# Performance work log

Hardware: AMD Instinct MI355X
Metric: run time of the kernel (lower is better)

The kernel has to match this reference:

```python
import jax, jax.numpy as jnp
import numpy as np

B, T, N, D = 8, 32, 24, 128          # batch, seq_len, max_node_num, roi_feature_size
H_LINK, H_LSTM, C, P = 128, 128, 6, 3  # link hidden, lstm hidden, big_attr_classes, propagate_layers


def setup_inputs() -> dict:
    key = jax.random.key(0)
    ks = jax.random.split(key, 20)
    node_num_rec = jax.random.randint(ks[0], (B, T), 2, N + 1)  # valid nodes per frame
    node_mask = jnp.arange(N)[None, None, :] < node_num_rec[:, :, None]          # [B,T,N]
    pair_mask = node_mask[:, :, :, None] & node_mask[:, :, None, :]              # [B,T,N,N]
    offdiag = ~jnp.eye(N, dtype=bool)
    # post-ResNet ROI features; invalid nodes / self-edges are zero (as in the torch code)
    node_resnet = jax.random.normal(ks[1], (B, T, D, N)) * node_mask[:, :, None, :]
    edge_resnet = jax.random.normal(ks[2], (B, T, D, N, N)) * (pair_mask & offdiag)[:, :, None]

    def w(k, shape, fan):
        return jax.random.normal(k, shape) / np.sqrt(fan)

    return dict(
        node_resnet=node_resnet, edge_resnet=edge_resnet,
        link_W1=w(ks[3], (H_LINK, D), D), link_b1=jnp.zeros((H_LINK,)),
        link_W2=w(ks[4], (1, H_LINK), H_LINK), link_b2=jnp.zeros((1,)),
        msg_Wh=w(ks[5], (D, D), 2 * D), msg_We=w(ks[6], (D, D), 2 * D), msg_b=jnp.zeros((D,)),
        gru_Wih=w(ks[7], (3 * D, D), D), gru_Whh=w(ks[8], (3 * D, D), D),
        gru_bih=jnp.zeros((3 * D,)), gru_bhh=jnp.zeros((3 * D,)),
        lstm_Wih=w(ks[9], (4 * H_LSTM, D), D), lstm_Whh=w(ks[10], (4 * H_LSTM, H_LSTM), H_LSTM),
        lstm_bih=jnp.zeros((4 * H_LSTM,)), lstm_bhh=jnp.zeros((4 * H_LSTM,)),
        ro_W=w(ks[11], (C, H_LSTM), H_LSTM), ro_b=jnp.zeros((C,)),
        node_num_rec=node_num_rec,
    )


def reference(node_resnet, edge_resnet, link_W1, link_b1, link_W2, link_b2,
              msg_Wh, msg_We, msg_b, gru_Wih, gru_Whh, gru_bih, gru_bhh,
              lstm_Wih, lstm_Whh, lstm_bih, lstm_bhh, ro_W, ro_b, node_num_rec):
    node_mask = jnp.arange(N)[None, None, :] < node_num_rec[:, :, None]      # [B,T,N]
    pair_mask = node_mask[:, :, :, None] & node_mask[:, :, None, :]          # [B,T,N,N]
    fmask_n = node_mask[:, :, None, :].astype(node_resnet.dtype)             # [B,T,1,N]
    fmask_p = pair_mask.astype(node_resnet.dtype)                            # [B,T,N,N]

    h_node = node_resnet      # [B,T,D,N]
    h_edge = edge_resnet      # [B,T,D,N,N]
    for _ in range(P):
        # link_fun (GraphConv = per-edge 1x1-conv MLP) -> adjacency logits, sigmoid gate on valid pairs
        hid = jax.nn.relu(jnp.einsum('btdvw,hd->bthvw', h_edge, link_W1)
                          + link_b1[None, None, :, None, None])
        adj = jnp.einsum('bthvw,h->btvw', hid, link_W2[0]) + link_b2[0]      # [B,T,N,N]
        gate = jax.nn.sigmoid(adj) * fmask_p
        # message_fun 'linear_concat_relu': relu(W @ concat(h_w, e_vw) + b), e_vw is raw edge feature
        msg = jax.nn.relu(jnp.einsum('btdw,od->btow', h_node, msg_Wh)[:, :, :, None, :]
                          + jnp.einsum('btdvw,od->btovw', edge_resnet, msg_We)
                          + msg_b[None, None, :, None, None])                # [B,T,D,N,N]
        gated = gate[:, :, None] * msg
        # hidden edge states of next round: gated messages in valid region, clone of edge feats elsewhere
        h_edge = jnp.where(pair_mask[:, :, None], gated, edge_resnet)
        m_v = jnp.sum(gated, axis=-1)                                        # [B,T,D,N] sum over senders
        # update_fun: single-step GRU, input m_v, hidden h_node
        x = m_v.transpose(0, 1, 3, 2)      # [B,T,N,D]
        h = h_node.transpose(0, 1, 3, 2)
        gi = x @ gru_Wih.T + gru_bih
        gh = h @ gru_Whh.T + gru_bhh
        i_r, i_z, i_n = jnp.split(gi, 3, axis=-1)
        h_r, h_z, h_n = jnp.split(gh, 3, axis=-1)
        r = jax.nn.sigmoid(i_r + h_r)
        z = jax.nn.sigmoid(i_z + h_z)
        n = jnp.tanh(i_n + r * h_n)
        h_new = ((1.0 - z) * n + z * h).transpose(0, 1, 3, 2)                # [B,T,D,N]
        h_node = jnp.where(node_mask[:, :, None, :], h_new, node_resnet)

    # temporal LSTM over seq dim; node (and batch) axis acts as LSTM batch, zero initial state
    x_seq = h_node.transpose(1, 0, 3, 2).reshape(T, B * N, D)
    h0 = jnp.zeros((B * N, H_LSTM), dtype=x_seq.dtype)
    c0 = jnp.zeros_like(h0)

    def cell(carry, xt):
        h, c = carry
        g = xt @ lstm_Wih.T + lstm_bih + h @ lstm_Whh.T + lstm_bhh
        i, f, gg, o = jnp.split(g, 4, axis=-1)
        c = jax.nn.sigmoid(f) * c + jax.nn.sigmoid(i) * jnp.tanh(gg)
        h = jax.nn.sigmoid(o) * jnp.tanh(c)
        return (h, c), h

    _, out = jax.lax.scan(cell, (h0, c0), x_seq)                             # [T,B*N,H]
    out = out.reshape(T, B, N, H_LSTM).transpose(1, 0, 2, 3)                 # [B,T,N,H]
    pred_label = (out @ ro_W.T + ro_b) * node_mask[..., None]                # [B,T,N,C]
    return pred_label
```

## Files before the change

### kernel.cpp

```cpp
#include <hip/hip_runtime.h>
#include <cmath>

typedef unsigned short u16;
typedef unsigned int   u32;
typedef short bf16x8 __attribute__((ext_vector_type(8)));
typedef float f32x4 __attribute__((ext_vector_type(4)));

constexpr int B_ = 8, T_ = 32, N_ = 24, D_ = 128;
constexpr int BT_ = B_ * T_;
constexpr int VW_ = N_ * N_;
constexpr int BTN_ = BT_ * N_;
constexpr int BTVW_ = BT_ * VW_;
constexpr int P_ = 3;
constexpr int C_ = 6;
constexpr int SA_ = 136;

__device__ __forceinline__ float bits2f(u32 u) { float f; __builtin_memcpy(&f, &u, 4); return f; }
__device__ __forceinline__ float bf2f(u16 h) { return bits2f(((u32)h) << 16); }
__device__ __forceinline__ u16 f2bf(float f) {
    u32 u; __builtin_memcpy(&u, &f, 4);
    u32 r = u + 0x7FFFu + ((u >> 16) & 1u);
    return (u16)(r >> 16);
}
__device__ __forceinline__ f32x4 ld4bf(const u16* p) {
    const uint2 v = *(const uint2*)p;
    f32x4 r;
    r[0] = bf2f((u16)v.x); r[1] = bf2f((u16)(v.x >> 16));
    r[2] = bf2f((u16)v.y); r[3] = bf2f((u16)(v.y >> 16));
    return r;
}
__device__ __forceinline__ float fexp2(float x) { return __builtin_amdgcn_exp2f(x); }
__device__ __forceinline__ float frcp(float x) { return __builtin_amdgcn_rcpf(x); }
__device__ __forceinline__ float sigm(float x) {
    return frcp(1.0f + fexp2(x * -1.4426950408889634f));
}
__device__ __forceinline__ float ftanh(float x) {
    const float t = fexp2(fabsf(x) * -2.8853900817779268f);
    return copysignf((1.0f - t) * frcp(1.0f + t), x);
}

struct CvtArgs {
    const void* src[10];
    u16* dst[10];
    int start[11];
};

__global__ __launch_bounds__(256) void k_convall(CvtArgs a) {
    const int idx = blockIdx.x * 256 + threadIdx.x;
    if (idx >= a.start[10]) return;
    int s = 0;
#pragma unroll
    for (int i = 1; i < 10; ++i) s += (idx >= a.start[i]) ? 1 : 0;
    const int off = idx - a.start[s];
    a.dst[s][off] = f2bf(((const float*)a.src[s])[off]);
}

struct FlArgs {
    const float* src[7];
    u16* dst[7];
    int start[8];
};

__global__ __launch_bounds__(256) void k_fraglin(FlArgs a) {
    const int idx = blockIdx.x * 256 + threadIdx.x;
    if (idx >= a.start[7]) return;
    int s = 0;
#pragma unroll
    for (int i = 1; i < 7; ++i) s += (idx >= a.start[i]) ? 1 : 0;
    const int off = idx - a.start[s];
    const int e = off & 7, lane = (off >> 3) & 63;
    const int ks = (off >> 9) & 3, rb = off >> 11;
    const int m = lane & 15, quad = lane >> 4;
    a.dst[s][off] = f2bf(a.src[s][(size_t)(rb * 16 + m) * 128 + ks * 32 + quad * 8 + e]);
}

__global__ __launch_bounds__(256) void k_transpose_node(const float* __restrict__ node,
                                                        float* __restrict__ HN,
                                                        u16* __restrict__ HNb) {
    const int bt = blockIdx.x;
    for (int f = threadIdx.x; f < 3072; f += 256) {
        const int d = f / 24, n = f - d * 24;
        const float v = node[(size_t)bt * 3072 + f];
        HN[(size_t)bt * 3072 + n * 128 + d] = v;
        HNb[(size_t)bt * 3072 + n * 128 + d] = f2bf(v);
    }
}

__global__ __launch_bounds__(64, 4) void k_prep(
    const float* __restrict__ edge, const u16* __restrict__ WeF,
    const u16* __restrict__ W1F, const u16* __restrict__ b1,
    const u16* __restrict__ W2, const u16* __restrict__ b2,
    u16* __restrict__ ME, float* __restrict__ ADJ) {
    __shared__ __align__(16) u16 A[32 * 128];
    const int tid = threadIdx.x;
    const int bt = blockIdx.x / 18, tile = blockIdx.x % 18;
    const int vw0 = tile * 32;
    const size_t ebase = (size_t)bt * D_ * VW_ + vw0;
    const int vq = tid & 7, dg = tid >> 3;
    u32* A32 = (u32*)A;
    {
        float4 fa[8], fb[8];
#pragma unroll
        for (int it = 0; it < 8; ++it) {
            const int d0 = it * 16 + dg * 2;
            fa[it] = *(const float4*)&edge[ebase + (size_t)d0 * VW_ + vq * 4];
            fb[it] = *(const float4*)&edge[ebase + (size_t)(d0 + 1) * VW_ + vq * 4];
        }
#pragma unroll
        for (int it = 0; it < 8; ++it) {
            const int d0 = it * 16 + dg * 2;
            const float* pa = (const float*)&fa[it];
            const float* pb = (const float*)&fb[it];
#pragma unroll
            for (int i = 0; i < 4; ++i) {
                const int row = vq * 4 + i;
                const int sw32 = ((row >> 2) & 7) * 4;
                A32[row * 64 + ((d0 >> 1) ^ sw32)] =
                    (u32)f2bf(pa[i]) | ((u32)f2bf(pb[i]) << 16);
            }
        }
    }
    __syncthreads();
    const int m = tid & 15, quad = tid >> 4;
    bf16x8 a[2][4];
#pragma unroll
    for (int rt = 0; rt < 2; ++rt) {
        const int row = rt * 16 + m;
        const int sw16 = ((row >> 2) & 7) * 8;
#pragma unroll
        for (int ks = 0; ks < 4; ++ks)
            a[rt][ks] = *(const bf16x8*)&A[row * 128 + ((ks * 32 + quad * 8) ^ sw16)];
    }
    const f32x4 z = {0.f, 0.f, 0.f, 0.f};
    float p[2][4] = {};
    const float b2v = bf2f(b2[0]);
#pragma unroll
    for (int ct = 0; ct < 8; ++ct) {
        bf16x8 bwe[4], bw1[4];
#pragma unroll
        for (int ks = 0; ks < 4; ++ks) {
            bwe[ks] = *(const bf16x8*)&WeF[((ct * 4 + ks) << 9) + tid * 8];
            bw1[ks] = *(const bf16x8*)&W1F[((ct * 4 + ks) << 9) + tid * 8];
        }
        f32x4 accE[2], accA[2];
#pragma unroll
        for (int rt = 0; rt < 2; ++rt) { accE[rt] = z; accA[rt] = z; }
#pragma unroll
        for (int rt = 0; rt < 2; ++rt)
#pragma unroll
            for (int ks = 0; ks < 4; ++ks) {
                accE[rt] = __builtin_amdgcn_mfma_f32_16x16x32_bf16(bwe[ks], a[rt][ks], accE[rt], 0, 0, 0);
                accA[rt] = __builtin_amdgcn_mfma_f32_16x16x32_bf16(a[rt][ks], bw1[ks], accA[rt], 0, 0, 0);
            }
#pragma unroll
        for (int rt = 0; rt < 2; ++rt) {
            const u32 lo = (u32)f2bf(accE[rt][0]) | ((u32)f2bf(accE[rt][1]) << 16);
            const u32 hi = (u32)f2bf(accE[rt][2]) | ((u32)f2bf(accE[rt][3]) << 16);
            *(uint2*)&ME[(size_t)(bt * VW_ + vw0 + rt * 16 + m) * 128 + ct * 16 + quad * 4] =
                make_uint2(lo, hi);
        }
        const int n = ct * 16 + m;
        const float b1v = bf2f(b1[n]);
        const float w2v = bf2f(W2[n]);
#pragma unroll
        for (int rt = 0; rt < 2; ++rt)
#pragma unroll
            for (int reg = 0; reg < 4; ++reg)
                p[rt][reg] += fmaxf(accA[rt][reg] + b1v, 0.0f) * w2v;
    }
#pragma unroll
    for (int rt = 0; rt < 2; ++rt)
#pragma unroll
        for (int reg = 0; reg < 4; ++reg) {
            float v = p[rt][reg];
            v += __shfl_xor(v, 1);
            v += __shfl_xor(v, 2);
            v += __shfl_xor(v, 4);
            v += __shfl_xor(v, 8);
            p[rt][reg] = v;
        }
    if (m == 0) {
#pragma unroll
        for (int rt = 0; rt < 2; ++rt)
#pragma unroll
            for (int reg = 0; reg < 4; ++reg)
                ADJ[bt * VW_ + vw0 + rt * 16 + quad * 4 + reg] = p[rt][reg] + b2v;
    }
}

template <bool ADJP>
__global__ __launch_bounds__(256) void k_fused(
    const u16* __restrict__ ME, const float* __restrict__ XW,
    const u16* __restrict__ mb,
    const u16* __restrict__ W1F, const u16* __restrict__ b1,
    const u16* __restrict__ W2, const u16* __restrict__ b2,
    const int* __restrict__ nnr, float* __restrict__ ADJ,
    u16* __restrict__ MVb) {
    __shared__ __align__(16) u16 A[48 * SA_];
    __shared__ float gate_s[48];
    __shared__ float2 mvp[2][2][64];
    const int tid = threadIdx.x;
    const int blk = blockIdx.x;
    const int bt = blk / 12, pr = blk - bt * 12;
    const int v0 = pr * 2;
    const int e0 = bt * VW_ + v0 * N_;
    const int nv = nnr[bt];

    if (tid < 48) gate_s[tid] = sigm(ADJ[e0 + tid]);
    __syncthreads();
    {
        const int op = tid & 63;
        const int sub = (tid >> 6) & 1;
        const int grp = tid >> 7;
        const int v = v0 + grp;
        const u32 mbu = ((const u32*)mb)[op];
        const float mb0 = bf2f((u16)mbu), mb1 = bf2f((u16)(mbu >> 16));
        const bool vva = v < nv;
        u32 meR[12]; float2 xwR[12];
#pragma unroll
        for (int i = 0; i < 12; ++i) {
            const int w = sub * 12 + i;
            const int rr = grp * 24 + w;
            meR[i] = ((const u32*)ME)[(size_t)(e0 + rr) * 64 + op];
            xwR[i] = *(const float2*)&XW[(size_t)(bt * N_ + w) * 128 + 2 * op];
        }
        float mvx = 0.0f, mvy = 0.0f;
        u32* A32 = (u32*)A;
#pragma unroll
        for (int i = 0; i < 12; ++i) {
            const int w = sub * 12 + i;
            const int rr = grp * 24 + w;
            float v0f = 0.0f, v1f = 0.0f;
            if (vva && w < nv) {
                const float g = gate_s[rr];
                v0f = g * fmaxf(xwR[i].x + bf2f((u16)meR[i]) + mb0, 0.0f);
                v1f = g * fmaxf(xwR[i].y + bf2f((u16)(meR[i] >> 16)) + mb1, 0.0f);
                mvx += v0f; mvy += v1f;
            }
            if (ADJP) A32[rr * 68 + op] = (u32)f2bf(v0f) | ((u32)f2bf(v1f) << 16);
        }
        mvp[grp][sub][op] = make_float2(mvx, mvy);
    }
    __syncthreads();
    if (tid < 128) {
        const int g2 = tid >> 6, o2 = tid & 63;
        const float2 pa = mvp[g2][0][o2], pb = mvp[g2][1][o2];
        ((u32*)MVb)[(size_t)(bt * N_ + v0 + g2) * 64 + o2] =
            (u32)f2bf(pa.x + pb.x) | ((u32)f2bf(pa.y + pb.y) << 16);
    }

    if constexpr (ADJP) {
        __syncthreads();
        if (tid >= 64) return;
        const int m = tid & 15, quad = tid >> 4;
        bf16x8 a[3][4];
#pragma unroll
        for (int rt = 0; rt < 3; ++rt)
#pragma unroll
            for (int ks = 0; ks < 4; ++ks)
                a[rt][ks] = *(const bf16x8*)&A[(rt * 16 + m) * SA_ + ks * 32 + quad * 8];
        const f32x4 z = {0.f, 0.f, 0.f, 0.f};
        float p[3][4] = {};
        const float b2v = bf2f(b2[0]);
#pragma unroll
        for (int ct = 0; ct < 8; ++ct) {
            bf16x8 bw[4];
#pragma unroll
            for (int ks = 0; ks < 4; ++ks)
                bw[ks] = *(const bf16x8*)&W1F[((ct * 4 + ks) << 9) + tid * 8];
            f32x4 acc[3];
#pragma unroll
            for (int rt = 0; rt < 3; ++rt) acc[rt] = z;
#pragma unroll
            for (int rt = 0; rt < 3; ++rt)
#pragma unroll
                for (int ks = 0; ks < 4; ++ks)
                    acc[rt] = __builtin_amdgcn_mfma_f32_16x16x32_bf16(a[rt][ks], bw[ks], acc[rt], 0, 0, 0);
            const int n = ct * 16 + m;
            const float b1v = bf2f(b1[n]);
            const float w2v = bf2f(W2[n]);
#pragma unroll
            for (int rt = 0; rt < 3; ++rt)
#pragma unroll
                for (int reg = 0; reg < 4; ++reg)
                    p[rt][reg] += fmaxf(acc[rt][reg] + b1v, 0.0f) * w2v;
        }
#pragma unroll
        for (int rt = 0; rt < 3; ++rt)
#pragma unroll
            for (int reg = 0; reg < 4; ++reg) {
                float v = p[rt][reg];
                v += __shfl_xor(v, 1);
                v += __shfl_xor(v, 2);
                v += __shfl_xor(v, 4);
                v += __shfl_xor(v, 8);
                p[rt][reg] = v;
            }
        if (m == 0) {
#pragma unroll
            for (int rt = 0; rt < 3; ++rt)
#pragma unroll
                for (int reg = 0; reg < 4; ++reg)
                    ADJ[e0 + rt * 16 + quad * 4 + reg] = p[rt][reg] + b2v;
        }
    }
}

__global__ __launch_bounds__(64, 1) void k_xw(const u16* __restrict__ HNb,
                                              const u16* __restrict__ WhF,
                                              float* __restrict__ XW) {
    const int tid = threadIdx.x;
    const int m = tid & 15, quad = tid >> 4;
    const int r0 = blockIdx.x * 16;
    const int ct0 = blockIdx.y * 4;
    bf16x8 a[4];
#pragma unroll
    for (int ks = 0; ks < 4; ++ks)
        a[ks] = *(const bf16x8*)&HNb[(size_t)(r0 + m) * 128 + ks * 32 + quad * 8];
    const f32x4 z = {0.f, 0.f, 0.f, 0.f};
#pragma unroll
    for (int cti = 0; cti < 4; ++cti) {
        const int ct = ct0 + cti;
        f32x4 acc = z;
#pragma unroll
        for (int ks = 0; ks < 4; ++ks) {
            const bf16x8 b = *(const bf16x8*)&WhF[((ct * 4 + ks) << 9) + tid * 8];
            acc = __builtin_amdgcn_mfma_f32_16x16x32_bf16(b, a[ks], acc, 0, 0, 0);
        }
        *(f32x4*)&XW[(size_t)(r0 + m) * 128 + ct * 16 + quad * 4] = acc;
    }
}

__global__ __launch_bounds__(64, 1) void k_gruM(
    const u16* __restrict__ MVb, const u16* __restrict__ HNb_in,
    float* __restrict__ HN, u16* __restrict__ HNb,
    const u16* __restrict__ WihF, const u16* __restrict__ WhhF,
    const u16* __restrict__ bih, const u16* __restrict__ bhh,
    const int* __restrict__ nnr) {
    const int tid = threadIdx.x;
    const int m = tid & 15, quad = tid >> 4;
    const int rbase = blockIdx.x * 16;
    const int ct0 = blockIdx.y * 4;
    bf16x8 amv[4], ahn[4];
#pragma unroll
    for (int ks = 0; ks < 4; ++ks) {
        amv[ks] = *(const bf16x8*)&MVb[(size_t)(rbase + m) * 128 + ks * 32 + quad * 8];
        ahn[ks] = *(const bf16x8*)&HNb_in[(size_t)(rbase + m) * 128 + ks * 32 + quad * 8];
    }
    const int myrow = rbase + m;
    const int mybt = myrow / N_;
    const bool valid = (myrow - mybt * N_) < nnr[mybt];
    const f32x4 z = {0.f, 0.f, 0.f, 0.f};
#pragma unroll
    for (int cti = 0; cti < 4; ++cti) {
        const int ct = ct0 + cti;
        f32x4 gi[3], gh[3];
#pragma unroll
        for (int g = 0; g < 3; ++g) { gi[g] = z; gh[g] = z; }
#pragma unroll
        for (int g = 0; g < 3; ++g) {
            const int rb = g * 8 + ct;
#pragma unroll
            for (int ks = 0; ks < 4; ++ks) {
                const bf16x8 bi_f = *(const bf16x8*)&WihF[((rb * 4 + ks) << 9) + tid * 8];
                const bf16x8 bh_f = *(const bf16x8*)&WhhF[((rb * 4 + ks) << 9) + tid * 8];
                gi[g] = __builtin_amdgcn_mfma_f32_16x16x32_bf16(bi_f, amv[ks], gi[g], 0, 0, 0);
                gh[g] = __builtin_amdgcn_mfma_f32_16x16x32_bf16(bh_f, ahn[ks], gh[g], 0, 0, 0);
            }
        }
        const int col0 = ct * 16 + quad * 4;
        const f32x4 biR = ld4bf(&bih[col0]),       bhR = ld4bf(&bhh[col0]);
        const f32x4 biZ = ld4bf(&bih[128 + col0]), bhZ = ld4bf(&bhh[128 + col0]);
        const f32x4 biN = ld4bf(&bih[256 + col0]), bhN = ld4bf(&bhh[256 + col0]);
        const size_t oi = (size_t)myrow * 128 + col0;
        const f32x4 hold = *(const f32x4*)&HN[oi];
        f32x4 hv;
#pragma unroll
        for (int reg = 0; reg < 4; ++reg) {
            const float r  = sigm(gi[0][reg] + gh[0][reg] + biR[reg] + bhR[reg]);
            const float zz = sigm(gi[1][reg] + gh[1][reg] + biZ[reg] + bhZ[reg]);
            const float nn = ftanh(gi[2][reg] + biN[reg] + r * (gh[2][reg] + bhN[reg]));
            hv[reg] = valid ? ((1.0f - zz) * nn + zz * hold[reg]) : 0.0f;
        }
        *(f32x4*)&HN[oi] = hv;
        const u32 lo = (u32)f2bf(hv[0]) | ((u32)f2bf(hv[1]) << 16);
        const u32 hi = (u32)f2bf(hv[2]) | ((u32)f2bf(hv[3]) << 16);
        *(uint2*)&HNb[oi] = make_uint2(lo, hi);
    }
}

__global__ __launch_bounds__(64, 2) void k_gi(const u16* __restrict__ HNb,
                                              const u16* __restrict__ WF,
                                              const u16* __restrict__ bih, const u16* __restrict__ bhh,
                                              float* __restrict__ GI2) {
    const int tid = threadIdx.x;
    const int m = tid & 15, quad = tid >> 4;
    const int r0 = blockIdx.x * 16;
    const int ocol0 = blockIdx.y * 128;
    const int r = r0 + m;
    const int btq = r / 24, n = r - btq * 24;
    const int b = btq >> 5, t = btq & 31;
    const int q = b * 24 + n;
    const int blk = q >> 4, mrow = q & 15;
    bf16x8 a[4];
#pragma unroll
    for (int ks = 0; ks < 4; ++ks)
        a[ks] = *(const bf16x8*)&HNb[(size_t)r * 128 + ks * 32 + quad * 8];
    const f32x4 z = {0.f, 0.f, 0.f, 0.f};
#pragma unroll
    for (int ct = 0; ct < 8; ++ct) {
        f32x4 acc = z;
        const int rb = blockIdx.y * 8 + ct;
#pragma unroll
        for (int ks = 0; ks < 4; ++ks) {
            const bf16x8 bb = *(const bf16x8*)&WF[((rb * 4 + ks) << 9) + tid * 8];
            acc = __builtin_amdgcn_mfma_f32_16x16x32_bf16(bb, a[ks], acc, 0, 0, 0);
        }
        const int col0 = ocol0 + ct * 16 + quad * 4;
        const f32x4 bi4 = ld4bf(&bih[col0]);
        const f32x4 bh4 = ld4bf(&bhh[col0]);
#pragma unroll
        for (int reg = 0; reg < 4; ++reg) acc[reg] += bi4[reg] + bh4[reg];
        const int cta = (ocol0 >> 4) + ct;
        const int w = cta & 7, j = cta >> 3;
        const size_t addr = ((size_t)(blk * 32 + t) * 512 + (w * 64 + quad * 16 + mrow)) * 16 + j * 4;
        *(f32x4*)&GI2[addr] = acc;
    }
}

__global__ __launch_bounds__(512) void k_rec(const float* __restrict__ GI2,
                                             const u16* __restrict__ WhhF,
                                             float* __restrict__ OUTH) {
    __shared__ __align__(16) u16 Abuf[2][16 * 128];
    const int tid = threadIdx.x;
    const int w = tid >> 6, lane = tid & 63;
    const int m = lane & 15, quad = lane >> 4;
    const int blk = blockIdx.x;
    const int q = blk * 16 + m;
    bf16x8 bw[4][4];
#pragma unroll
    for (int j = 0; j < 4; ++j)
#pragma unroll
        for (int ks = 0; ks < 4; ++ks)
            bw[j][ks] = *(const bf16x8*)&WhhF[(((j * 8 + w) * 4 + ks) << 9) + lane * 8];
    const f32x4 z = {0.f, 0.f, 0.f, 0.f};
    f32x4 cst = z;
    bf16x8 a[4];
#pragma unroll
    for (int ks = 0; ks < 4; ++ks) a[ks] = (bf16x8)(short)0;
    const float* gb = GI2 + ((size_t)blk * 32 * 512 + tid) * 16;
    f32x4 g[4], gn[4];
#pragma unroll
    for (int j = 0; j < 4; ++j) g[j] = *(const f32x4*)&gb[j * 4];
    const int ws = w * 2 + (quad >> 1);
    const int woff = (quad & 1) * 2;
    for (int t = 0; t < T_; ++t) {
        const int tn = (t + 1 < T_) ? (t + 1) : (T_ - 1);
        const size_t gnb = (size_t)tn * 512 * 16;
#pragma unroll
        for (int j = 0; j < 4; ++j) gn[j] = *(const f32x4*)&gb[gnb + j * 4];
        f32x4 acc[4];
#pragma unroll
        for (int j = 0; j < 4; ++j) acc[j] = z;
#pragma unroll
        for (int j = 0; j < 4; ++j)
#pragma unroll
            for (int ks = 0; ks < 4; ++ks)
                acc[j] = __builtin_amdgcn_mfma_f32_16x16x32_bf16(bw[j][ks], a[ks], acc[j], 0, 0, 0);
        f32x4 hv;
#pragma unroll
        for (int r = 0; r < 4; ++r) {
            const float gi_ = acc[0][r] + g[0][r];
            const float gf_ = acc[1][r] + g[1][r];
            const float gg_ = acc[2][r] + g[2][r];
            const float go_ = acc[3][r] + g[3][r];
            cst[r] = sigm(gf_) * cst[r] + sigm(gi_) * ftanh(gg_);
            hv[r] = sigm(go_) * ftanh(cst[r]);
        }
        *(f32x4*)&OUTH[((size_t)t * 192 + q) * 128 + w * 16 + quad * 4] = hv;
        const u32 lo = (u32)f2bf(hv[0]) | ((u32)f2bf(hv[1]) << 16);
        const u32 hi = (u32)f2bf(hv[2]) | ((u32)f2bf(hv[3]) << 16);
        u32* dst = (u32*)&Abuf[(t + 1) & 1][0];
        *(uint2*)&dst[m * 64 + ((ws ^ m) << 2) + woff] = make_uint2(lo, hi);
        __syncthreads();
        const u16* src = &Abuf[(t + 1) & 1][0];
#pragma unroll
        for (int ks = 0; ks < 4; ++ks)
            a[ks] = *(const bf16x8*)&src[m * 128 + (((ks * 4 + quad) ^ m) << 3)];
#pragma unroll
        for (int j = 0; j < 4; ++j) g[j] = gn[j];
    }
}

__global__ __launch_bounds__(256) void k_readout(const float* __restrict__ OUTH,
                                                 const u16* __restrict__ roW,
                                                 const u16* __restrict__ rob,
                                                 const int* __restrict__ nnr,
                                                 float* __restrict__ out) {
    const int idx = blockIdx.x * 256 + threadIdx.x;
    const int btn = idx / C_, c = idx - btn * C_;
    const int bt = btn / N_, n = btn - bt * N_;
    const int b = bt / T_, t = bt - b * T_;
    const int nv = nnr[bt];
    float val = 0.0f;
    if (n < nv) {
        const float* hrow = OUTH + ((size_t)t * 192 + b * N_ + n) * 128;
        const uint2* w2 = (const uint2*)&roW[c * 128];
        float acc = bf2f(rob[c]);
#pragma unroll
        for (int k4 = 0; k4 < 32; ++k4) {
            const float4 h4 = *(const float4*)&hrow[k4 * 4];
            const uint2 ww = w2[k4];
            acc = fmaf(bf2f((u16)ww.x), h4.x,
                  fmaf(bf2f((u16)(ww.x >> 16)), h4.y,
                  fmaf(bf2f((u16)ww.y), h4.z,
                  fmaf(bf2f((u16)(ww.y >> 16)), h4.w, acc))));
        }
        val = acc;
    }
    out[idx] = val;
}

extern "C" void kernel_launch(void* const* d_in, const int* in_sizes, int n_in,
                              void* d_out, int out_size, void* d_ws, size_t ws_size,
                              hipStream_t stream) {
    const float* node = (const float*)d_in[0];
    const float* edge = (const float*)d_in[1];
    const int* nnr = (const int*)d_in[19];

    char* ws = (char*)d_ws;
    float* HN = (float*)ws;   ws += (size_t)BTN_ * D_ * 4;
    u16* HNb = (u16*)ws;      ws += (size_t)BTN_ * D_ * 2;
    float* XW = (float*)ws;   ws += (size_t)BTN_ * D_ * 4;
    u16* MVb = (u16*)ws;      ws += (size_t)BTN_ * D_ * 2;
    float* ADJ = (float*)ws;  ws += (size_t)BTVW_ * 4;
    float* GI = (float*)ws;   ws += (size_t)BTN_ * 512 * 4;
    u16* WThh = (u16*)ws;     ws += 65536 * 2;
    u16* ME = (u16*)ws;       ws += (size_t)BTVW_ * D_ * 2;
    float* OUTH = XW;

    u16* cbase = (u16*)ws;
    const int cvtN17[17] = {16384, 128, 128, 1, 16384, 16384, 128,
                            49152, 49152, 384, 384, 65536, 65536, 512, 512, 768, 6};
    u16* cptr[17];
    {
        int off = 0;
        for (int i = 0; i < 17; ++i) {
            cptr[i] = cbase + off;
            off += (cvtN17[i] + 7) & ~7;
        }
    }
    CvtArgs ca;
    {
        const int din_idx[10] = {3, 4, 5, 8, 11, 12, 15, 16, 17, 18};
        const int slot[10]    = {1, 2, 3, 6,  9, 10, 13, 14, 15, 16};
        const int nelem[10]   = {128, 128, 1, 128, 384, 384, 512, 512, 768, 6};
        int cum = 0;
        for (int i = 0; i < 10; ++i) {
            ca.src[i] = d_in[din_idx[i]];
            ca.dst[i] = cptr[slot[i]];
            ca.start[i] = cum;
            cum += nelem[i];
        }
        ca.start[10] = cum;
    }
    FlArgs fa;
    {
        const int din_idx[7] = {2, 6, 7, 9, 10, 13, 14};
        const int slot[7]    = {0, 4, 5, 7,  8, 11, 12};
        const int nelem[7]   = {16384, 16384, 16384, 49152, 49152, 65536, 65536};
        int cum = 0;
        for (int i = 0; i < 7; ++i) {
            fa.src[i] = (const float*)d_in[din_idx[i]];
            fa.dst[i] = cptr[slot[i]];
            fa.start[i] = cum;
            cum += nelem[i];
        }
        fa.start[7] = cum;
    }
    u16* fW1 = cptr[0];  u16* cb1 = cptr[1];  u16* cW2 = cptr[2];  u16* cb2 = cptr[3];
    u16* fWh = cptr[4];  u16* fWe = cptr[5];  u16* cmb = cptr[6];
    u16* fgWih = cptr[7]; u16* fgWhh = cptr[8]; u16* cgbih = cptr[9]; u16* cgbhh = cptr[10];
    u16* flsWih = cptr[11]; u16* flsWhh = cptr[12]; u16* clsbih = cptr[13]; u16* clsbhh = cptr[14];
    u16* croW = cptr[15]; u16* crob = cptr[16];
    (void)WThh;

    k_convall<<<12, 256, 0, stream>>>(ca);
    k_fraglin<<<1088, 256, 0, stream>>>(fa);
    k_transpose_node<<<BT_, 256, 0, stream>>>(node, HN, HNb);
    k_prep<<<BT_ * 18, 64, 0, stream>>>(edge, fWe, fW1, cb1, cW2, cb2, ME, ADJ);
    for (int l = 0; l < P_; ++l) {
        k_xw<<<dim3(384, 2), 64, 0, stream>>>(HNb, fWh, XW);
        if (l < P_ - 1)
            k_fused<true><<<BTN_ / 2, 256, 0, stream>>>(ME, XW, cmb, fW1, cb1, cW2, cb2,
                                                        nnr, ADJ, MVb);
        else
            k_fused<false><<<BTN_ / 2, 256, 0, stream>>>(ME, XW, cmb, fW1, cb1, cW2, cb2,
                                                         nnr, ADJ, MVb);
        k_gruM<<<dim3(384, 2), 64, 0, stream>>>(MVb, HNb, HN, HNb, fgWih, fgWhh, cgbih, cgbhh, nnr);
    }
    k_gi<<<dim3(384, 4), 64, 0, stream>>>(HNb, flsWih, clsbih, clsbhh, GI);
    k_rec<<<12, 512, 0, stream>>>(GI, flsWhh, OUTH);
    k_readout<<<144, 256, 0, stream>>>(OUTH, croW, crob, nnr, (float*)d_out);
}
```

Measured before the change: 349.2 us.

## Merge preprocessing kernels, split k_prep loops with prefetch, double grid for GEMM kernels

Three preprocessing launches (weight conversion, fragment linearization, node transpose) are merged into one kernel that dispatches on block index, removing two launches. In k_prep the interleaved edge-message and link-MLP MFMA loops become two sequential loops with register double-buffered weight prefetch, which lowers live accumulator and weight registers. k_xw, k_gruM and k_gi each handle half as many column tiles per block while their grids double, adding parallelism at the cost of reloading the A fragments in more blocks.

```diff
diff --git a/kernel.cpp b/kernel.cpp
--- a/kernel.cpp
+++ b/kernel.cpp
@@ -39,50 +39,41 @@
     return copysignf((1.0f - t) * frcp(1.0f + t), x);
 }
 
-struct CvtArgs {
-    const void* src[10];
-    u16* dst[10];
-    int start[11];
+struct PreArgs {
+    const float* node; float* HN; u16* HNb;
+    const float* fsrc[7]; u16* fdst[7]; int fstart[8];
+    const void* csrc[10]; u16* cdst[10]; int cstart[11];
 };
 
-__global__ __launch_bounds__(256) void k_convall(CvtArgs a) {
-    const int idx = blockIdx.x * 256 + threadIdx.x;
-    if (idx >= a.start[10]) return;
-    int s = 0;
-#pragma unroll
-    for (int i = 1; i < 10; ++i) s += (idx >= a.start[i]) ? 1 : 0;
-    const int off = idx - a.start[s];
-    a.dst[s][off] = f2bf(((const float*)a.src[s])[off]);
-}
-
-struct FlArgs {
-    const float* src[7];
-    u16* dst[7];
-    int start[8];
-};
-
-__global__ __launch_bounds__(256) void k_fraglin(FlArgs a) {
-    const int idx = blockIdx.x * 256 + threadIdx.x;
-    if (idx >= a.start[7]) return;
-    int s = 0;
-#pragma unroll
-    for (int i = 1; i < 7; ++i) s += (idx >= a.start[i]) ? 1 : 0;
-    const int off = idx - a.start[s];
-    const int e = off & 7, lane = (off >> 3) & 63;
-    const int ks = (off >> 9) & 3, rb = off >> 11;
-    const int m = lane & 15, quad = lane >> 4;
-    a.dst[s][off] = f2bf(a.src[s][(size_t)(rb * 16 + m) * 128 + ks * 32 + quad * 8 + e]);
-}
-
-__global__ __launch_bounds__(256) void k_transpose_node(const float* __restrict__ node,
-                                                        float* __restrict__ HN,
-                                                        u16* __restrict__ HNb) {
-    const int bt = blockIdx.x;
-    for (int f = threadIdx.x; f < 3072; f += 256) {
-        const int d = f / 24, n = f - d * 24;
-        const float v = node[(size_t)bt * 3072 + f];
-        HN[(size_t)bt * 3072 + n * 128 + d] = v;
-        HNb[(size_t)bt * 3072 + n * 128 + d] = f2bf(v);
+__global__ __launch_bounds__(256) void k_preproc(PreArgs a) {
+    const int bx = blockIdx.x;
+    if (bx < 256) {
+        const int bt = bx;
+        for (int f = threadIdx.x; f < 3072; f += 256) {
+            const int d = f / 24, n = f - d * 24;
+            const float v = a.node[(size_t)bt * 3072 + f];
+            a.HN[(size_t)bt * 3072 + n * 128 + d] = v;
+            a.HNb[(size_t)bt * 3072 + n * 128 + d] = f2bf(v);
+        }
+    } else if (bx < 1344) {
+        const int idx = (bx - 256) * 256 + threadIdx.x;
+        if (idx >= a.fstart[7]) return;
+        int s = 0;
+#pragma unroll
+        for (int i = 1; i < 7; ++i) s += (idx >= a.fstart[i]) ? 1 : 0;
+        const int off = idx - a.fstart[s];
+        const int e = off & 7, lane = (off >> 3) & 63;
+        const int ks = (off >> 9) & 3, rb = off >> 11;
+        const int m = lane & 15, quad = lane >> 4;
+        a.fdst[s][off] = f2bf(a.fsrc[s][(size_t)(rb * 16 + m) * 128 + ks * 32 + quad * 8 + e]);
+    } else {
+        const int idx = (bx - 1344) * 256 + threadIdx.x;
+        if (idx >= a.cstart[10]) return;
+        int s = 0;
+#pragma unroll
+        for (int i = 1; i < 10; ++i) s += (idx >= a.cstart[i]) ? 1 : 0;
+        const int off = idx - a.cstart[s];
+        a.cdst[s][off] = f2bf(((const float*)a.csrc[s])[off]);
     }
 }
 
@@ -132,33 +123,53 @@
             a[rt][ks] = *(const bf16x8*)&A[row * 128 + ((ks * 32 + quad * 8) ^ sw16)];
     }
     const f32x4 z = {0.f, 0.f, 0.f, 0.f};
+    bf16x8 bwc[4], bwn[4];
+#pragma unroll
+    for (int ks = 0; ks < 4; ++ks)
+        bwc[ks] = *(const bf16x8*)&WeF[(ks << 9) + tid * 8];
+#pragma unroll
+    for (int ct = 0; ct < 8; ++ct) {
+#pragma unroll
+        for (int ks = 0; ks < 4; ++ks) {
+            const u16* src = (ct < 7) ? &WeF[(((ct + 1) * 4 + ks) << 9) + tid * 8]
+                                      : &W1F[(ks << 9) + tid * 8];
+            bwn[ks] = *(const bf16x8*)src;
+        }
+        f32x4 acc[2];
+#pragma unroll
+        for (int rt = 0; rt < 2; ++rt) acc[rt] = z;
+#pragma unroll
+        for (int rt = 0; rt < 2; ++rt)
+#pragma unroll
+            for (int ks = 0; ks < 4; ++ks)
+                acc[rt] = __builtin_amdgcn_mfma_f32_16x16x32_bf16(bwc[ks], a[rt][ks], acc[rt], 0, 0, 0);
+#pragma unroll
+        for (int rt = 0; rt < 2; ++rt) {
+            const u32 lo = (u32)f2bf(acc[rt][0]) | ((u32)f2bf(acc[rt][1]) << 16);
+            const u32 hi = (u32)f2bf(acc[rt][2]) | ((u32)f2bf(acc[rt][3]) << 16);
+            *(uint2*)&ME[(size_t)(bt * VW_ + vw0 + rt * 16 + m) * 128 + ct * 16 + quad * 4] =
+                make_uint2(lo, hi);
+        }
+#pragma unroll
+        for (int ks = 0; ks < 4; ++ks) bwc[ks] = bwn[ks];
+    }
     float p[2][4] = {};
     const float b2v = bf2f(b2[0]);
 #pragma unroll
     for (int ct = 0; ct < 8; ++ct) {
-        bf16x8 bwe[4], bw1[4];
-#pragma unroll
-        for (int ks = 0; ks < 4; ++ks) {
-            bwe[ks] = *(const bf16x8*)&WeF[((ct * 4 + ks) << 9) + tid * 8];
-            bw1[ks] = *(const bf16x8*)&W1F[((ct * 4 + ks) << 9) + tid * 8];
-        }
-        f32x4 accE[2], accA[2];
-#pragma unroll
-        for (int rt = 0; rt < 2; ++rt) { accE[rt] = z; accA[rt] = z; }
+        if (ct < 7) {
+#pragma unroll
+            for (int ks = 0; ks < 4; ++ks)
+                bwn[ks] = *(const bf16x8*)&W1F[(((ct + 1) * 4 + ks) << 9) + tid * 8];
+        }
+        f32x4 acc[2];
+#pragma unroll
+        for (int rt = 0; rt < 2; ++rt) acc[rt] = z;
 #pragma unroll
         for (int rt = 0; rt < 2; ++rt)
 #pragma unroll
-            for (int ks = 0; ks < 4; ++ks) {
-                accE[rt] = __builtin_amdgcn_mfma_f32_16x16x32_bf16(bwe[ks], a[rt][ks], accE[rt], 0, 0, 0);
-                accA[rt] = __builtin_amdgcn_mfma_f32_16x16x32_bf16(a[rt][ks], bw1[ks], accA[rt], 0, 0, 0);
-            }
-#pragma unroll
-        for (int rt = 0; rt < 2; ++rt) {
-            const u32 lo = (u32)f2bf(accE[rt][0]) | ((u32)f2bf(accE[rt][1]) << 16);
-            const u32 hi = (u32)f2bf(accE[rt][2]) | ((u32)f2bf(accE[rt][3]) << 16);
-            *(uint2*)&ME[(size_t)(bt * VW_ + vw0 + rt * 16 + m) * 128 + ct * 16 + quad * 4] =
-                make_uint2(lo, hi);
-        }
+            for (int ks = 0; ks < 4; ++ks)
+                acc[rt] = __builtin_amdgcn_mfma_f32_16x16x32_bf16(a[rt][ks], bwc[ks], acc[rt], 0, 0, 0);
         const int n = ct * 16 + m;
         const float b1v = bf2f(b1[n]);
         const float w2v = bf2f(W2[n]);
@@ -166,7 +177,11 @@
         for (int rt = 0; rt < 2; ++rt)
 #pragma unroll
             for (int reg = 0; reg < 4; ++reg)
-                p[rt][reg] += fmaxf(accA[rt][reg] + b1v, 0.0f) * w2v;
+                p[rt][reg] += fmaxf(acc[rt][reg] + b1v, 0.0f) * w2v;
+        if (ct < 7) {
+#pragma unroll
+            for (int ks = 0; ks < 4; ++ks) bwc[ks] = bwn[ks];
+        }
     }
 #pragma unroll
     for (int rt = 0; rt < 2; ++rt)
@@ -312,14 +327,14 @@
     const int tid = threadIdx.x;
     const int m = tid & 15, quad = tid >> 4;
     const int r0 = blockIdx.x * 16;
-    const int ct0 = blockIdx.y * 4;
+    const int ct0 = blockIdx.y * 2;
     bf16x8 a[4];
 #pragma unroll
     for (int ks = 0; ks < 4; ++ks)
         a[ks] = *(const bf16x8*)&HNb[(size_t)(r0 + m) * 128 + ks * 32 + quad * 8];
     const f32x4 z = {0.f, 0.f, 0.f, 0.f};
 #pragma unroll
-    for (int cti = 0; cti < 4; ++cti) {
+    for (int cti = 0; cti < 2; ++cti) {
         const int ct = ct0 + cti;
         f32x4 acc = z;
 #pragma unroll
@@ -340,7 +355,7 @@
     const int tid = threadIdx.x;
     const int m = tid & 15, quad = tid >> 4;
     const int rbase = blockIdx.x * 16;
-    const int ct0 = blockIdx.y * 4;
+    const int ct0 = blockIdx.y * 2;
     bf16x8 amv[4], ahn[4];
 #pragma unroll
     for (int ks = 0; ks < 4; ++ks) {
@@ -352,7 +367,7 @@
     const bool valid = (myrow - mybt * N_) < nnr[mybt];
     const f32x4 z = {0.f, 0.f, 0.f, 0.f};
 #pragma unroll
-    for (int cti = 0; cti < 4; ++cti) {
+    for (int cti = 0; cti < 2; ++cti) {
         const int ct = ct0 + cti;
         f32x4 gi[3], gh[3];
 #pragma unroll
@@ -396,7 +411,7 @@
     const int tid = threadIdx.x;
     const int m = tid & 15, quad = tid >> 4;
     const int r0 = blockIdx.x * 16;
-    const int ocol0 = blockIdx.y * 128;
+    const int ocol0 = blockIdx.y * 64;
     const int r = r0 + m;
     const int btq = r / 24, n = r - btq * 24;
     const int b = btq >> 5, t = btq & 31;
@@ -408,9 +423,9 @@
         a[ks] = *(const bf16x8*)&HNb[(size_t)r * 128 + ks * 32 + quad * 8];
     const f32x4 z = {0.f, 0.f, 0.f, 0.f};
 #pragma unroll
-    for (int ct = 0; ct < 8; ++ct) {
+    for (int ct = 0; ct < 4; ++ct) {
         f32x4 acc = z;
-        const int rb = blockIdx.y * 8 + ct;
+        const int rb = blockIdx.y * 4 + ct;
 #pragma unroll
         for (int ks = 0; ks < 4; ++ks) {
             const bf16x8 bb = *(const bf16x8*)&WF[((rb * 4 + ks) << 9) + tid * 8];
@@ -550,33 +565,33 @@
             off += (cvtN17[i] + 7) & ~7;
         }
     }
-    CvtArgs ca;
+    PreArgs pa;
+    pa.node = node; pa.HN = HN; pa.HNb = HNb;
+    {
+        const int din_idx[7] = {2, 6, 7, 9, 10, 13, 14};
+        const int slot[7]    = {0, 4, 5, 7,  8, 11, 12};
+        const int nelem[7]   = {16384, 16384, 16384, 49152, 49152, 65536, 65536};
+        int cum = 0;
+        for (int i = 0; i < 7; ++i) {
+            pa.fsrc[i] = (const float*)d_in[din_idx[i]];
+            pa.fdst[i] = cptr[slot[i]];
+            pa.fstart[i] = cum;
+            cum += nelem[i];
+        }
+        pa.fstart[7] = cum;
+    }
     {
         const int din_idx[10] = {3, 4, 5, 8, 11, 12, 15, 16, 17, 18};
         const int slot[10]    = {1, 2, 3, 6,  9, 10, 13, 14, 15, 16};
         const int nelem[10]   = {128, 128, 1, 128, 384, 384, 512, 512, 768, 6};
         int cum = 0;
         for (int i = 0; i < 10; ++i) {
-            ca.src[i] = d_in[din_idx[i]];
-            ca.dst[i] = cptr[slot[i]];
-            ca.start[i] = cum;
+            pa.csrc[i] = d_in[din_idx[i]];
+            pa.cdst[i] = cptr[slot[i]];
+            pa.cstart[i] = cum;
             cum += nelem[i];
         }
-        ca.start[10] = cum;
-    }
-    FlArgs fa;
-    {
-        const int din_idx[7] = {2, 6, 7, 9, 10, 13, 14};
-        const int slot[7]    = {0, 4, 5, 7,  8, 11, 12};
-        const int nelem[7]   = {16384, 16384, 16384, 49152, 49152, 65536, 65536};
-        int cum = 0;
-        for (int i = 0; i < 7; ++i) {
-            fa.src[i] = (const float*)d_in[din_idx[i]];
-            fa.dst[i] = cptr[slot[i]];
-            fa.start[i] = cum;
-            cum += nelem[i];
-        }
-        fa.start[7] = cum;
+        pa.cstart[10] = cum;
     }
     u16* fW1 = cptr[0];  u16* cb1 = cptr[1];  u16* cW2 = cptr[2];  u16* cb2 = cptr[3];
     u16* fWh = cptr[4];  u16* fWe = cptr[5];  u16* cmb = cptr[6];
@@ -585,21 +600,19 @@
     u16* croW = cptr[15]; u16* crob = cptr[16];
     (void)WThh;
 
-    k_convall<<<12, 256, 0, stream>>>(ca);
-    k_fraglin<<<1088, 256, 0, stream>>>(fa);
-    k_transpose_node<<<BT_, 256, 0, stream>>>(node, HN, HNb);
+    k_preproc<<<1356, 256, 0, stream>>>(pa);
     k_prep<<<BT_ * 18, 64, 0, stream>>>(edge, fWe, fW1, cb1, cW2, cb2, ME, ADJ);
     for (int l = 0; l < P_; ++l) {
-        k_xw<<<dim3(384, 2), 64, 0, stream>>>(HNb, fWh, XW);
+        k_xw<<<dim3(384, 4), 64, 0, stream>>>(HNb, fWh, XW);
         if (l < P_ - 1)
             k_fused<true><<<BTN_ / 2, 256, 0, stream>>>(ME, XW, cmb, fW1, cb1, cW2, cb2,
                                                         nnr, ADJ, MVb);
         else
             k_fused<false><<<BTN_ / 2, 256, 0, stream>>>(ME, XW, cmb, fW1, cb1, cW2, cb2,
                                                          nnr, ADJ, MVb);
-        k_gruM<<<dim3(384, 2), 64, 0, stream>>>(MVb, HNb, HN, HNb, fgWih, fgWhh, cgbih, cgbhh, nnr);
-    }
-    k_gi<<<dim3(384, 4), 64, 0, stream>>>(HNb, flsWih, clsbih, clsbhh, GI);
+        k_gruM<<<dim3(384, 4), 64, 0, stream>>>(MVb, HNb, HN, HNb, fgWih, fgWhh, cgbih, cgbhh, nnr);
+    }
+    k_gi<<<dim3(384, 8), 64, 0, stream>>>(HNb, flsWih, clsbih, clsbhh, GI);
     k_rec<<<12, 512, 0, stream>>>(GI, flsWhh, OUTH);
     k_readout<<<144, 256, 0, stream>>>(OUTH, croW, crob, nnr, (float*)d_out);
 }
```

Result: faster. 339.0 us (-2.9%).
